# Kernel optimization log

Measured on AMD Instinct MI355X. Metric: run time of the kernel, lower is better.

## Reference

```python
import jax, jax.numpy as jnp
import numpy as np

DIM, FFN, GC, NSET, K = 48, 2, 2, 32, 3
HID = DIM * FFN          # 96 hidden features
G = HID // GC            # 48 groups in KBA
CG = HID // G            # 2 channels per group
INTERC = 24              # min(dim, 24)
B, H, W = 4, 128, 128


def _conv(x, w, b=None, groups=1, pad=0):
    out = jax.lax.conv_general_dilated(
        x, w, (1, 1), [(pad, pad), (pad, pad)],
        dimension_numbers=('NCHW', 'OIHW', 'NCHW'),
        feature_group_count=groups)
    if b is not None:
        out = out + b[None, :, None, None]
    return out


def _kba(x, att, k, g, bb, ww):
    # x: [B,c,H,W], att: [B,nset,H,W], bb: [1,nset,c], ww: [1,nset,c*c//g*k*k]
    Bz, c, Hh, Ww = x.shape
    KK = k * k
    cg = c // g
    P = Hh * Ww
    a = att.reshape(Bz, -1, P).transpose(0, 2, 1)                     # [B,P,nset]
    bias = jnp.einsum('bpn,nc->bpc', a, bb[0])                        # [B,P,c]
    attk = jnp.einsum('bpn,nm->bpm', a, ww[0]).reshape(Bz, P, g, cg, cg * KK)
    pd = k // 2
    xp = jnp.pad(x, ((0, 0), (0, 0), (pd, pd), (pd, pd)))
    # im2col patches, torch.unfold layout: channel-major, kernel row-major
    patches = jnp.stack([xp[:, :, i:i + Hh, j:j + Ww]
                         for i in range(k) for j in range(k)], axis=2)  # [B,c,KK,H,W]
    uf = patches.reshape(Bz, g, cg * KK, P).transpose(0, 3, 1, 2)       # [B,P,g,cg*KK]
    out = jnp.einsum('bpgom,bpgm->bpgo', attk, uf).reshape(Bz, P, c) + bias
    return out.transpose(0, 2, 1).reshape(Bz, c, Hh, Ww)


def setup_inputs() -> dict:
    key = jax.random.key(0)
    ks = jax.random.split(key, 20)
    s = 0.05
    inp = {
        'x': jax.random.normal(ks[0], (B, DIM, H, W), jnp.float32),
        'dw1_w': jax.random.normal(ks[1], (HID, DIM, 1, 1), jnp.float32) * s,
        'dw2_w': jax.random.normal(ks[2], (HID, 1, 3, 3), jnp.float32) * s,
        'proj_w': jax.random.normal(ks[3], (DIM, HID, 1, 1), jnp.float32) * s,
        'sca_w': jax.random.normal(ks[4], (HID, HID, 1, 1), jnp.float32) * s,
        'sca_b': jax.random.normal(ks[5], (HID,), jnp.float32) * s,
        'c1_w1': jax.random.normal(ks[6], (HID, DIM, 1, 1), jnp.float32) * s,
        'c1_w2': jax.random.normal(ks[7], (HID, 1, 3, 3), jnp.float32) * s,
        'kba_w': jax.random.normal(ks[8], (1, NSET, HID * CG * K * K), jnp.float32) * s,
        'kba_b': jax.random.normal(ks[9], (1, NSET, HID), jnp.float32) * s,
        'c2_w1': jax.random.normal(ks[10], (INTERC, DIM // INTERC, 3, 3), jnp.float32) * s,
        'c2_b1': jax.random.normal(ks[11], (INTERC,), jnp.float32) * s,
        'c2_w2': jax.random.normal(ks[12], (NSET, INTERC // 2, 1, 1), jnp.float32) * s,
        'c2_b2': jax.random.normal(ks[13], (NSET,), jnp.float32) * s,
        'c211_w': jax.random.normal(ks[14], (NSET, DIM, 1, 1), jnp.float32) * s,
        'c211_b': jax.random.normal(ks[15], (NSET,), jnp.float32) * s,
        'attgamma': jnp.full((1, NSET, 1, 1), 0.01, jnp.float32),
        'ga1': jnp.full((1, HID, 1, 1), 0.01, jnp.float32),
    }
    return inp


def reference(x, dw1_w, dw2_w, proj_w, sca_w, sca_b, c1_w1, c1_w2,
              kba_w, kba_b, c2_w1, c2_b1, c2_w2, c2_b2,
              c211_w, c211_b, attgamma, ga1):
    # dwconv branch: 1x1 -> depthwise 3x3
    x1 = _conv(_conv(x, dw1_w), dw2_w, groups=HID, pad=1)
    # attention map branch: grouped 3x3 -> SimpleGate -> 1x1, scaled + skip 1x1
    t = _conv(x, c2_w1, c2_b1, groups=INTERC, pad=1)
    t1, t2 = jnp.split(t, 2, axis=1)
    t = _conv(t1 * t2, c2_w2, c2_b2)
    att = t * attgamma + _conv(x, c211_w, c211_b)
    # conv1 branch feeding KBA
    uf = _conv(_conv(x, c1_w1), c1_w2, groups=HID, pad=1)
    x2 = _kba(uf, att, K, G, kba_b, kba_w) * ga1 + uf
    comb = jax.nn.gelu(x1, approximate=False) * x2
    pooled = jnp.mean(comb, axis=(2, 3), keepdims=True)
    comb = comb * _conv(pooled, sca_w, sca_b)
    return _conv(comb, proj_w)
```

## Files before the change

### kernel.cpp

```cpp
#include <hip/hip_runtime.h>
#include <math.h>

#define BB 4
#define HH 128
#define WW 128
#define HWP (HH*WW)
#define DIMC 48
#define HIDC 96
#define NSETC 32

typedef __attribute__((ext_vector_type(8))) short bf16x8;
typedef __attribute__((ext_vector_type(4))) float f32x4;
typedef __attribute__((ext_vector_type(2))) float f32x2;

static __device__ __forceinline__ unsigned short f2bf(float f) {
    union { float f; unsigned u; } v; v.f = f;
    unsigned r = (v.u + 0x7FFFu + ((v.u >> 16) & 1u)) >> 16;
    return (unsigned short)r;
}
static __device__ __forceinline__ unsigned rnd_bf(float f) {
    union { float f; unsigned u; } v; v.f = f;
    return v.u + 0x8000u;
}
static __device__ __forceinline__ unsigned pack2bf(float lo, float hi) {
    return __builtin_amdgcn_perm(rnd_bf(hi), rnd_bf(lo), 0x07060302u);
}
static __device__ __forceinline__ void st_bf_hi(unsigned short* p, float f) {
    *p = (unsigned short)(rnd_bf(f) >> 16);
}
static __device__ __forceinline__ float bf2f(unsigned short u) {
    union { unsigned u; float f; } v; v.u = ((unsigned)u) << 16;
    return v.f;
}
static __device__ __forceinline__ float bfpair_lo(unsigned pr) {
    union { unsigned u; float f; } v; v.u = pr << 16; return v.f;
}
static __device__ __forceinline__ float bfpair_hi(unsigned pr) {
    union { unsigned u; float f; } v; v.u = pr & 0xffff0000u; return v.f;
}
static __device__ __forceinline__ float gelu(float x) {
    return 0.5f * x * (1.0f + erff(x * 0.70710678118654752f));
}

__global__ __launch_bounds__(256) void k_prep(
    const float* __restrict__ x,
    const float* __restrict__ kbaw, const float* __restrict__ kbab,
    const float* __restrict__ dw1w, const float* __restrict__ c1w1,
    const float* __restrict__ ga1,  const float* __restrict__ c211w,
    const float* __restrict__ c2w2, const float* __restrict__ c2b2,
    const float* __restrict__ c211b, const float* __restrict__ attg,
    unsigned short* __restrict__ Bpk, unsigned short* __restrict__ Bpw,
    unsigned short* __restrict__ Aps, unsigned short* __restrict__ Ag,
    unsigned* __restrict__ x_p, float* __restrict__ pooled)
{
    __shared__ unsigned ts[256 * 26];
    int blk = blockIdx.x, tid = threadIdx.x;
    if (blk < 300) {
        int t = blk * 256 + tid;
        if (t < 61440) {
            int j = t & 7, lane = (t >> 3) & 63, tile = t >> 9;
            int chunk = tile / 10, nt = tile - chunk * 10;
            int m = lane & 15, qn = lane >> 4;
            int lc = 4 * nt + (m & 3);
            int o = lc / 20, tt = lc % 20;
            int c = (m >> 2) * 24 + 2 * chunk + o;
            int n = qn * 8 + j;
            float v = 0.f;
            if (tt < 18)       v = kbaw[n * 1728 + (c >> 1) * 36 + (c & 1) * 18 + tt] * ga1[c];
            else if (tt == 18) v = kbab[n * 96 + c] * ga1[c];
            Bpk[t] = f2bf(v);
        } else if (t < 73728) {
            int u = t - 61440;
            int s = u / 6144;
            int rem = u % 6144;
            int nt = rem >> 9;
            int lane = (rem >> 3) & 63, j = rem & 7;
            int k = s * 32 + ((lane >> 4) << 3) + j;
            int col = (nt << 4) + (lane & 15);
            float v = 0.f;
            if (k < 48) v = (col < 96) ? dw1w[col * 48 + k] : c1w1[(col - 96) * 48 + k];
            Bpw[u] = f2bf(v);
        } else if (t < 75776) {
            int u = t - 73728;
            int j = u & 7, lane = (u >> 3) & 63, tile = u >> 9;
            int kt = tile >> 1, nt2 = tile & 1;
            int m = lane & 15, qn = lane >> 4;
            int n = 8 * (m >> 2) + 4 * nt2 + (m & 3);
            int k = kt * 32 + qn * 8 + j;
            Aps[u] = f2bf(k < 48 ? c211w[n * 48 + k] : 0.f);
        } else if (t < 76800) {
            int u = t - 75776;
            int j = u & 7, lane = (u >> 3) & 63, nt2 = u >> 9;
            int m = lane & 15, qn = lane >> 4;
            int n = 8 * (m >> 2) + 4 * nt2 + (m & 3);
            int k = qn * 8 + j;
            float v = 0.f;
            if (k < 12)       v = c2w2[n * 12 + k] * attg[n];
            else if (k == 12) v = c2b2[n] * attg[n] + c211b[n];
            Ag[u] = f2bf(v);
        }
    } else {
        int xblk = blk - 300;
        if (xblk == 0) {
            for (int i = tid; i < BB * HIDC; i += 256) pooled[i] = 0.f;
        }
        int b = xblk >> 6;
        int p0 = (xblk & 63) << 8;
        const float* xb = x + (size_t)b * DIMC * HWP + p0;
        #pragma unroll
        for (int c2 = 0; c2 < 24; ++c2) {
            float lo = xb[(2 * c2) * HWP + tid];
            float hi = xb[(2 * c2 + 1) * HWP + tid];
            ts[tid * 26 + c2] = pack2bf(lo, hi);
        }
        __syncthreads();
        unsigned* dst = x_p + ((size_t)b * HWP + p0) * 24;
        for (int idx = tid; idx < 256 * 24; idx += 256) {
            int px = idx / 24, j2 = idx - px * 24;
            dst[px * 24 + j2] = ts[px * 26 + j2];
        }
    }
}

__global__ __launch_bounds__(512, 4) void k_mff(
    const unsigned* __restrict__ x_p,
    const uint4* __restrict__ BpkA, const uint4* __restrict__ Bpw,
    const uint4* __restrict__ Aps,  const uint4* __restrict__ Ag,
    const float* __restrict__ c1w2, const float* __restrict__ dw2w,
    const float* __restrict__ c2w1, const float* __restrict__ c2b1,
    unsigned* __restrict__ comb_bf, float* __restrict__ pooled)
{
    __shared__ __attribute__((aligned(16))) unsigned xs[144 * 26];
    __shared__ __attribute__((aligned(16))) unsigned short hsw[144 * 100];
    __shared__ unsigned short us2p[100 * 100];
    __shared__ float wls[864 + 432 + 24];
    __shared__ float pooled_s[96];

    int lane = threadIdx.x, wy = threadIdx.y;
    int tid = wy * 64 + lane;
    int blk = blockIdx.x;
    int b = blk >> 8, ty = (blk >> 4) & 15, tx = blk & 15;
    int q = lane >> 4, i16 = lane & 15;
    int wh = wy >> 2;
    int wp = wy & 3;

    float* wats  = wls + 864;
    float* c2b1s = wls + 864 + 432;
    float* att_tf = (float*)hsw;

    if (tid < 96) pooled_s[tid] = 0.f;
    for (int idx = tid; idx < 864; idx += 512) {
        int t5 = idx / 96, c = idx - t5 * 96;
        wls[idx] = dw2w[c * 9 + t5];
    }
    for (int idx = tid; idx < 216; idx += 512) {
        int g = idx / 9, tap = idx - g * 9;
        wats[idx * 2]     = c2w1[g * 18 + tap];
        wats[idx * 2 + 1] = c2w1[g * 18 + 9 + tap];
    }
    if (tid < 24) c2b1s[tid] = c2b1[tid];
    for (int idx = tid; idx < 144 * 12; idx += 512) {
        int pos = idx / 12, jp = idx - pos * 12;
        int gy = ty * 8 - 2 + pos / 12, gx = tx * 8 - 2 + pos % 12;
        uint2 v = {0u, 0u};
        if (((unsigned)gy < (unsigned)HH) & ((unsigned)gx < (unsigned)WW))
            v = *(const uint2*)&x_p[((size_t)b * HWP + gy * WW + gx) * 24 + jp * 2];
        *(uint2*)&xs[pos * 26 + jp * 2] = v;
    }
    __syncthreads();

    int p_t = wp * 16 + i16;
    int pyT = p_t >> 3, pxT = p_t & 7;
    int gp = (ty * 8 + pyT) * WW + tx * 8 + pxT;
    uint4 z4 = {0u, 0u, 0u, 0u};

    #pragma unroll
    for (int ci = 0; ci < 3; ++ci) {
        int g = q * 6 + wh * 3 + ci;
        float acc = c2b1s[g];
        #pragma unroll
        for (int di = 0; di < 3; ++di)
          #pragma unroll
          for (int dj = 0; dj < 3; ++dj) {
              unsigned pr = xs[((pyT + 1 + di) * 12 + pxT + 1 + dj) * 26 + g];
              f32x2 w2 = *(const f32x2*)&wats[(g * 9 + di * 3 + dj) * 2];
              acc += w2.x * bfpair_lo(pr) + w2.y * bfpair_hi(pr);
          }
        att_tf[p_t * 26 + g] = acc;
    }
    __syncthreads();

    bf16x8 afrag;
    {
        int p26 = p_t * 26;
        unsigned tgd[4];
        #pragma unroll
        for (int i2 = 0; i2 < 4; ++i2) {
            int k0 = q * 8 + 2 * i2;
            int k1 = k0 + 1;
            float v0 = (k0 < 12) ? att_tf[p26 + k0] * att_tf[p26 + 12 + k0] : (k0 == 12 ? 1.f : 0.f);
            float v1 = (k1 < 12) ? att_tf[p26 + k1] * att_tf[p26 + 12 + k1] : (k1 == 12 ? 1.f : 0.f);
            tgd[i2] = pack2bf(v0, v1);
        }
        uint4 tgr = {tgd[0], tgd[1], tgd[2], tgd[3]};
        bf16x8 btg = __builtin_bit_cast(bf16x8, tgr);

        int cen = (pyT + 2) * 12 + (pxT + 2);
        uint2 xa = *(const uint2*)&xs[cen * 26 + q * 4];
        uint2 xb2 = *(const uint2*)&xs[cen * 26 + q * 4 + 2];
        uint4 bx0r = {xa.x, xa.y, xb2.x, xb2.y};
        uint4 bx1r = z4;
        if (q < 2) {
            uint2 xc = *(const uint2*)&xs[cen * 26 + 16 + q * 4];
            uint2 xd = *(const uint2*)&xs[cen * 26 + 16 + q * 4 + 2];
            bx1r.x = xc.x; bx1r.y = xc.y; bx1r.z = xd.x; bx1r.w = xd.y;
        }
        bf16x8 bx0 = __builtin_bit_cast(bf16x8, bx0r);
        bf16x8 bx1 = __builtin_bit_cast(bf16x8, bx1r);

        float attv[8];
        #pragma unroll
        for (int nt2 = 0; nt2 < 2; ++nt2) {
            bf16x8 ag  = __builtin_bit_cast(bf16x8, Ag[nt2 * 64 + lane]);
            bf16x8 as0 = __builtin_bit_cast(bf16x8, Aps[nt2 * 64 + lane]);
            bf16x8 as1 = __builtin_bit_cast(bf16x8, Aps[(2 + nt2) * 64 + lane]);
            f32x4 z = {0.f, 0.f, 0.f, 0.f};
            f32x4 c = __builtin_amdgcn_mfma_f32_16x16x32_bf16(ag, btg, z, 0, 0, 0);
            c = __builtin_amdgcn_mfma_f32_16x16x32_bf16(as1, bx1, c, 0, 0, 0);
            c = __builtin_amdgcn_mfma_f32_16x16x32_bf16(as0, bx0, c, 0, 0, 0);
            #pragma unroll
            for (int r = 0; r < 4; ++r) attv[nt2 * 4 + r] = c[r];
        }
        uint4 au = {pack2bf(attv[0], attv[1]), pack2bf(attv[2], attv[3]),
                    pack2bf(attv[4], attv[5]), pack2bf(attv[6], attv[7])};
        afrag = __builtin_bit_cast(bf16x8, au);
    }
    __syncthreads();

    {
        int nA = (wy == 0) ? 2 : 1;
        #pragma unroll 1
        for (int rr = 0; rr < nA; ++rr) {
            int rg = rr ? 8 : wy;
            int hp = rg * 16 + i16;
            uint2 xa = *(const uint2*)&xs[hp * 26 + q * 4];
            uint2 xb2 = *(const uint2*)&xs[hp * 26 + q * 4 + 2];
            uint4 a0r = {xa.x, xa.y, xb2.x, xb2.y};
            uint4 a1r = z4;
            if (q < 2) {
                uint2 xc = *(const uint2*)&xs[hp * 26 + 16 + q * 4];
                uint2 xd = *(const uint2*)&xs[hp * 26 + 16 + q * 4 + 2];
                a1r.x = xc.x; a1r.y = xc.y; a1r.z = xd.x; a1r.w = xd.y;
            }
            bf16x8 a0 = __builtin_bit_cast(bf16x8, a0r);
            bf16x8 a1 = __builtin_bit_cast(bf16x8, a1r);
            int rowb = rg * 16 + 4 * q;
            #pragma unroll
            for (int nt = 0; nt < 6; ++nt) {
                bf16x8 b0 = __builtin_bit_cast(bf16x8, Bpw[(size_t)((6 + nt) << 6) + lane]);
                bf16x8 b1 = __builtin_bit_cast(bf16x8, Bpw[(size_t)((18 + nt) << 6) + lane]);
                f32x4 z = {0.f, 0.f, 0.f, 0.f};
                f32x4 c = __builtin_amdgcn_mfma_f32_16x16x32_bf16(a1, b1, z, 0, 0, 0);
                c = __builtin_amdgcn_mfma_f32_16x16x32_bf16(a0, b0, c, 0, 0, 0);
                #pragma unroll
                for (int r = 0; r < 4; ++r)
                    st_bf_hi(&hsw[(rowb + r) * 100 + nt * 16 + i16], c[r]);
            }
        }
    }
    __syncthreads();

    #pragma unroll 1
    for (int it = 0; it < 3; ++it) {
        int su = wy * 3 + it;
        int cq = su >> 1;
        const float* w9 = c1w2 + cq * 8 * 9;
        int hp2 = (su & 1) * 50 + lane;
        if (lane < 50) {
            int py2 = hp2 / 10, px2 = hp2 - py2 * 10;
            float acc[8];
            #pragma unroll
            for (int c = 0; c < 8; ++c) acc[c] = 0.f;
            #pragma unroll
            for (int di = 0; di < 3; ++di)
              #pragma unroll
              for (int dj = 0; dj < 3; ++dj) {
                  int row = (py2 + di) * 12 + px2 + dj;
                  uint2 v0 = *(const uint2*)&hsw[row * 100 + cq * 8];
                  uint2 v1 = *(const uint2*)&hsw[row * 100 + cq * 8 + 4];
                  unsigned pp[4] = {v0.x, v0.y, v1.x, v1.y};
                  #pragma unroll
                  for (int c2 = 0; c2 < 4; ++c2) {
                      acc[2*c2]   += w9[(2*c2) * 9 + di * 3 + dj]   * bfpair_lo(pp[c2]);
                      acc[2*c2+1] += w9[(2*c2+1) * 9 + di * 3 + dj] * bfpair_hi(pp[c2]);
                  }
              }
            uint2 o0, o1;
            o0.x = pack2bf(acc[0], acc[1]);
            o0.y = pack2bf(acc[2], acc[3]);
            o1.x = pack2bf(acc[4], acc[5]);
            o1.y = pack2bf(acc[6], acc[7]);
            *(uint2*)&us2p[hp2 * 100 + cq * 8]     = o0;
            *(uint2*)&us2p[hp2 * 100 + cq * 8 + 4] = o1;
        }
    }
    __syncthreads();

    if (wy < 7) {
        int rg = wy;
        int hp = rg * 16 + i16;
        bool okp = hp < 100;
        int hy = hp / 10, hx = hp - hy * 10;
        int pos = okp ? ((hy + 1) * 12 + hx + 1) : 0;
        uint2 xa = *(const uint2*)&xs[pos * 26 + q * 4];
        uint2 xb2 = *(const uint2*)&xs[pos * 26 + q * 4 + 2];
        uint4 a0r = {xa.x, xa.y, xb2.x, xb2.y};
        uint4 a1r = z4;
        if (q < 2) {
            uint2 xc = *(const uint2*)&xs[pos * 26 + 16 + q * 4];
            uint2 xd = *(const uint2*)&xs[pos * 26 + 16 + q * 4 + 2];
            a1r.x = xc.x; a1r.y = xc.y; a1r.z = xd.x; a1r.w = xd.y;
        }
        bf16x8 a0 = __builtin_bit_cast(bf16x8, a0r);
        bf16x8 a1 = __builtin_bit_cast(bf16x8, a1r);
        int rowb = rg * 16 + 4 * q;
        #pragma unroll
        for (int nt = 0; nt < 6; ++nt) {
            bf16x8 b0 = __builtin_bit_cast(bf16x8, Bpw[(size_t)(nt << 6) + lane]);
            bf16x8 b1 = __builtin_bit_cast(bf16x8, Bpw[(size_t)((12 + nt) << 6) + lane]);
            f32x4 z = {0.f, 0.f, 0.f, 0.f};
            f32x4 c = __builtin_amdgcn_mfma_f32_16x16x32_bf16(a1, b1, z, 0, 0, 0);
            c = __builtin_amdgcn_mfma_f32_16x16x32_bf16(a0, b0, c, 0, 0, 0);
            #pragma unroll
            for (int r = 0; r < 4; ++r)
                st_bf_hi(&hsw[(rowb + r) * 100 + nt * 16 + i16], c[r]);
        }
    }
    __syncthreads();

    f32x2 greg[6];
    {
        int base = q * 24 + wh * 12;
        #pragma unroll
        for (int cc = 0; cc < 6; ++cc) {
            int c0 = base + 2 * cc;
            f32x2 acc = {0.f, 0.f};
            #pragma unroll
            for (int di = 0; di < 3; ++di)
              #pragma unroll
              for (int dj = 0; dj < 3; ++dj) {
                  unsigned pr = *(const unsigned*)&hsw[((pyT + di) * 10 + pxT + dj) * 100 + c0];
                  f32x2 hv = {bfpair_lo(pr), bfpair_hi(pr)};
                  f32x2 wv = *(const f32x2*)&wls[(di * 3 + dj) * 96 + c0];
                  acc += wv * hv;
              }
            greg[cc].x = gelu(acc.x);
            greg[cc].y = gelu(acc.y);
        }
    }

    unsigned* cmb = comb_bf + ((size_t)b * HWP + gp) * 48 + q * 12;
    int hpC = (pyT + 1) * 10 + pxT + 1;

    #pragma unroll
    for (int cl = 0; cl < 6; ++cl) {
        int chunk = wh * 6 + cl;
        f32x4 cf[10];
        #pragma unroll
        for (int nt = 0; nt < 10; ++nt) {
            bf16x8 aW = __builtin_bit_cast(bf16x8, BpkA[(size_t)((chunk * 10 + nt) << 6) + lane]);
            f32x4 z = {0.f, 0.f, 0.f, 0.f};
            cf[nt] = __builtin_amdgcn_mfma_f32_16x16x32_bf16(aW, afrag, z, 0, 0, 0);
        }
        int c0 = q * 24 + 2 * chunk;
        float u[18];
        #pragma unroll
        for (int i = 0; i < 3; ++i)
          #pragma unroll
          for (int j = 0; j < 3; ++j) {
              unsigned pr = *(const unsigned*)&us2p[((pyT + i) * 10 + pxT + j) * 100 + c0];
              u[i * 3 + j]     = bfpair_lo(pr);
              u[9 + i * 3 + j] = bfpair_hi(pr);
          }
        float acc0 = cf[4][2];
        float acc1 = cf[9][2];
        #pragma unroll
        for (int m = 0; m < 16; ++m) {
            acc0 += cf[m >> 2][m & 3]       * u[m];
            acc1 += cf[5 + (m >> 2)][m & 3] * u[m];
        }
        acc0 += cf[4][0] * u[16] + cf[4][1] * u[17];
        acc1 += cf[9][0] * u[16] + cf[9][1] * u[17];

        unsigned sp = *(const unsigned*)&us2p[hpC * 100 + c0];
        float x20 = acc0 + bfpair_lo(sp);
        float x21 = acc1 + bfpair_hi(sp);
        float cv0 = greg[cl].x * x20;
        float cv1 = greg[cl].y * x21;
        cmb[chunk] = pack2bf(cv0, cv1);
        float r0 = cv0, r1 = cv1;
        #pragma unroll
        for (int s = 1; s < 16; s <<= 1) {
            r0 += __shfl_xor(r0, s, 64);
            r1 += __shfl_xor(r1, s, 64);
        }
        if (i16 == 0) {
            atomicAdd(&pooled_s[c0], r0);
            atomicAdd(&pooled_s[c0 + 1], r1);
        }
    }
    __syncthreads();
    if (tid < 96) atomicAdd(&pooled[b * HIDC + tid], pooled_s[tid]);
}

__global__ __launch_bounds__(256) void k_final(
    const unsigned* __restrict__ comb_bf, const float* __restrict__ pooled,
    const float* __restrict__ scaw, const float* __restrict__ scab,
    const float* __restrict__ projw, float* __restrict__ out)
{
    __shared__ float svs[96];
    __shared__ float cs[96][66];
    int tid = threadIdx.x;
    int blk = blockIdx.x;
    int p0 = blk * 64;
    int b = p0 >> 14;
    if (tid < 96) {
        float dot = 0.f;
        const float* pr = pooled + b * 96;
        const float* wr = scaw + tid * 96;
        #pragma unroll 4
        for (int k = 0; k < 96; ++k) dot += wr[k] * pr[k];
        svs[tid] = scab[tid] + dot * (1.0f / (float)HWP);
    }
    __syncthreads();
    for (int idx = tid; idx < 64 * 12; idx += 256) {
        int px = idx / 12, cq = idx - px * 12;
        uint4 v = *(const uint4*)&comb_bf[(size_t)(p0 + px) * 48 + cq * 4];
        int k0 = cq * 8;
        unsigned pp[4] = {v.x, v.y, v.z, v.w};
        #pragma unroll
        for (int j = 0; j < 4; ++j) {
            cs[k0 + 2*j][px]     = bfpair_lo(pp[j]) * svs[k0 + 2*j];
            cs[k0 + 2*j + 1][px] = bfpair_hi(pp[j]) * svs[k0 + 2*j + 1];
        }
    }
    __syncthreads();
    int l = tid & 63, w = tid >> 6;
    int o0 = w * 12;
    float acc[12];
    #pragma unroll
    for (int o = 0; o < 12; ++o) acc[o] = 0.f;
    #pragma unroll 4
    for (int k = 0; k < 96; ++k) {
        float v = cs[k][l];
        #pragma unroll
        for (int o = 0; o < 12; ++o)
            acc[o] += projw[(o0 + o) * 96 + k] * v;
    }
    float* ob = out + (size_t)b * DIMC * HWP + (p0 & 16383) + l;
    #pragma unroll
    for (int o = 0; o < 12; ++o)
        ob[(o0 + o) * HWP] = acc[o];
}

extern "C" void kernel_launch(void* const* d_in, const int* in_sizes, int n_in,
                              void* d_out, int out_size, void* d_ws, size_t ws_size,
                              hipStream_t stream)
{
    const float* x     = (const float*)d_in[0];
    const float* dw1w  = (const float*)d_in[1];
    const float* dw2w  = (const float*)d_in[2];
    const float* projw = (const float*)d_in[3];
    const float* scaw  = (const float*)d_in[4];
    const float* scab  = (const float*)d_in[5];
    const float* c1w1  = (const float*)d_in[6];
    const float* c1w2  = (const float*)d_in[7];
    const float* kbaw  = (const float*)d_in[8];
    const float* kbab  = (const float*)d_in[9];
    const float* c2w1  = (const float*)d_in[10];
    const float* c2b1  = (const float*)d_in[11];
    const float* c2w2  = (const float*)d_in[12];
    const float* c2b2  = (const float*)d_in[13];
    const float* c211w = (const float*)d_in[14];
    const float* c211b = (const float*)d_in[15];
    const float* attg  = (const float*)d_in[16];
    const float* ga1   = (const float*)d_in[17];

    unsigned* x_p     = (unsigned*)d_ws;
    unsigned* comb_bf = x_p + (size_t)BB * HWP * 24;
    float* pooled     = (float*)(comb_bf + (size_t)BB * HWP * 48);
    unsigned short* BpkA = (unsigned short*)(pooled + BB * HIDC);
    unsigned short* Bpw  = BpkA + 61440;
    unsigned short* Aps  = Bpw + 12288;
    unsigned short* Ag   = Aps + 2048;

    k_prep <<<556,  256, 0, stream>>>(x, kbaw, kbab, dw1w, c1w1, ga1, c211w, c2w2, c2b2,
                                      c211b, attg, BpkA, Bpw, Aps, Ag, x_p, pooled);
    k_mff  <<<1024, dim3(64,8,1), 0, stream>>>(x_p, (const uint4*)BpkA, (const uint4*)Bpw,
                                               (const uint4*)Aps, (const uint4*)Ag,
                                               c1w2, dw2w, c2w1, c2b1, comb_bf, pooled);
    k_final<<<1024, 256, 0, stream>>>(comb_bf, pooled, scaw, scab, projw, (float*)d_out);
}
```

Before: 206.1 us.

## Pad shared-memory row strides to odd words and relax launch bounds

Changes the LDS row strides (xs 26→27 words, hsw/us2p 100→102 halves, i.e. 51 words) to avoid bank conflicts, replacing the vector uint2 LDS accesses with scalar 32-bit accesses that the new alignment requires. It lowers the launch-bounds minimum blocks from 4 to 2, giving the compiler more registers per thread at possible occupancy cost. It also hoists the us2p neighbourhood loads ahead of the MFMA batch so LDS latency overlaps the matrix ops. The risk is more LDS instructions from the scalarized accesses, plus lower occupancy.

New measurement: 200.8 us. -2.5%, faster.

```diff
diff --git a/kernel.cpp b/kernel.cpp
--- a/kernel.cpp
+++ b/kernel.cpp
@@ -8,6 +8,10 @@
 #define DIMC 48
 #define HIDC 96
 #define NSETC 32
+
+#define XS_W 27
+#define HS_W 102
+#define US_W 102
 
 typedef __attribute__((ext_vector_type(8))) short bf16x8;
 typedef __attribute__((ext_vector_type(4))) float f32x4;
@@ -122,7 +126,7 @@
     }
 }
 
-__global__ __launch_bounds__(512, 4) void k_mff(
+__global__ __launch_bounds__(512, 2) void k_mff(
     const unsigned* __restrict__ x_p,
     const uint4* __restrict__ BpkA, const uint4* __restrict__ Bpw,
     const uint4* __restrict__ Aps,  const uint4* __restrict__ Ag,
@@ -130,9 +134,9 @@
     const float* __restrict__ c2w1, const float* __restrict__ c2b1,
     unsigned* __restrict__ comb_bf, float* __restrict__ pooled)
 {
-    __shared__ __attribute__((aligned(16))) unsigned xs[144 * 26];
-    __shared__ __attribute__((aligned(16))) unsigned short hsw[144 * 100];
-    __shared__ unsigned short us2p[100 * 100];
+    __shared__ __attribute__((aligned(16))) unsigned xs[144 * XS_W];
+    __shared__ __attribute__((aligned(16))) unsigned short hsw[144 * HS_W];
+    __shared__ unsigned short us2p[100 * US_W];
     __shared__ float wls[864 + 432 + 24];
     __shared__ float pooled_s[96];
 
@@ -165,7 +169,8 @@
         uint2 v = {0u, 0u};
         if (((unsigned)gy < (unsigned)HH) & ((unsigned)gx < (unsigned)WW))
             v = *(const uint2*)&x_p[((size_t)b * HWP + gy * WW + gx) * 24 + jp * 2];
-        *(uint2*)&xs[pos * 26 + jp * 2] = v;
+        xs[pos * XS_W + jp * 2]     = v.x;
+        xs[pos * XS_W + jp * 2 + 1] = v.y;
     }
     __syncthreads();
 
@@ -182,17 +187,17 @@
         for (int di = 0; di < 3; ++di)
           #pragma unroll
           for (int dj = 0; dj < 3; ++dj) {
-              unsigned pr = xs[((pyT + 1 + di) * 12 + pxT + 1 + dj) * 26 + g];
+              unsigned pr = xs[((pyT + 1 + di) * 12 + pxT + 1 + dj) * XS_W + g];
               f32x2 w2 = *(const f32x2*)&wats[(g * 9 + di * 3 + dj) * 2];
               acc += w2.x * bfpair_lo(pr) + w2.y * bfpair_hi(pr);
           }
-        att_tf[p_t * 26 + g] = acc;
+        att_tf[p_t * XS_W + g] = acc;
     }
     __syncthreads();
 
     bf16x8 afrag;
     {
-        int p26 = p_t * 26;
+        int p26 = p_t * XS_W;
         unsigned tgd[4];
         #pragma unroll
         for (int i2 = 0; i2 < 4; ++i2) {
@@ -206,14 +211,12 @@
         bf16x8 btg = __builtin_bit_cast(bf16x8, tgr);
 
         int cen = (pyT + 2) * 12 + (pxT + 2);
-        uint2 xa = *(const uint2*)&xs[cen * 26 + q * 4];
-        uint2 xb2 = *(const uint2*)&xs[cen * 26 + q * 4 + 2];
-        uint4 bx0r = {xa.x, xa.y, xb2.x, xb2.y};
+        int cb = cen * XS_W + q * 4;
+        uint4 bx0r = {xs[cb], xs[cb + 1], xs[cb + 2], xs[cb + 3]};
         uint4 bx1r = z4;
         if (q < 2) {
-            uint2 xc = *(const uint2*)&xs[cen * 26 + 16 + q * 4];
-            uint2 xd = *(const uint2*)&xs[cen * 26 + 16 + q * 4 + 2];
-            bx1r.x = xc.x; bx1r.y = xc.y; bx1r.z = xd.x; bx1r.w = xd.y;
+            int cb2 = cen * XS_W + 16 + q * 4;
+            bx1r.x = xs[cb2]; bx1r.y = xs[cb2 + 1]; bx1r.z = xs[cb2 + 2]; bx1r.w = xs[cb2 + 3];
         }
         bf16x8 bx0 = __builtin_bit_cast(bf16x8, bx0r);
         bf16x8 bx1 = __builtin_bit_cast(bf16x8, bx1r);
@@ -243,14 +246,12 @@
         for (int rr = 0; rr < nA; ++rr) {
             int rg = rr ? 8 : wy;
             int hp = rg * 16 + i16;
-            uint2 xa = *(const uint2*)&xs[hp * 26 + q * 4];
-            uint2 xb2 = *(const uint2*)&xs[hp * 26 + q * 4 + 2];
-            uint4 a0r = {xa.x, xa.y, xb2.x, xb2.y};
+            int ab = hp * XS_W + q * 4;
+            uint4 a0r = {xs[ab], xs[ab + 1], xs[ab + 2], xs[ab + 3]};
             uint4 a1r = z4;
             if (q < 2) {
-                uint2 xc = *(const uint2*)&xs[hp * 26 + 16 + q * 4];
-                uint2 xd = *(const uint2*)&xs[hp * 26 + 16 + q * 4 + 2];
-                a1r.x = xc.x; a1r.y = xc.y; a1r.z = xd.x; a1r.w = xd.y;
+                int ab2 = hp * XS_W + 16 + q * 4;
+                a1r.x = xs[ab2]; a1r.y = xs[ab2 + 1]; a1r.z = xs[ab2 + 2]; a1r.w = xs[ab2 + 3];
             }
             bf16x8 a0 = __builtin_bit_cast(bf16x8, a0r);
             bf16x8 a1 = __builtin_bit_cast(bf16x8, a1r);
@@ -264,7 +265,7 @@
                 c = __builtin_amdgcn_mfma_f32_16x16x32_bf16(a0, b0, c, 0, 0, 0);
                 #pragma unroll
                 for (int r = 0; r < 4; ++r)
-                    st_bf_hi(&hsw[(rowb + r) * 100 + nt * 16 + i16], c[r]);
+                    st_bf_hi(&hsw[(rowb + r) * HS_W + nt * 16 + i16], c[r]);
             }
         }
     }
@@ -285,23 +286,23 @@
             for (int di = 0; di < 3; ++di)
               #pragma unroll
               for (int dj = 0; dj < 3; ++dj) {
-                  int row = (py2 + di) * 12 + px2 + dj;
-                  uint2 v0 = *(const uint2*)&hsw[row * 100 + cq * 8];
-                  uint2 v1 = *(const uint2*)&hsw[row * 100 + cq * 8 + 4];
-                  unsigned pp[4] = {v0.x, v0.y, v1.x, v1.y};
+                  int rb = ((py2 + di) * 12 + px2 + dj) * HS_W + cq * 8;
+                  unsigned pp[4];
+                  pp[0] = *(const unsigned*)&hsw[rb];
+                  pp[1] = *(const unsigned*)&hsw[rb + 2];
+                  pp[2] = *(const unsigned*)&hsw[rb + 4];
+                  pp[3] = *(const unsigned*)&hsw[rb + 6];
                   #pragma unroll
                   for (int c2 = 0; c2 < 4; ++c2) {
                       acc[2*c2]   += w9[(2*c2) * 9 + di * 3 + dj]   * bfpair_lo(pp[c2]);
                       acc[2*c2+1] += w9[(2*c2+1) * 9 + di * 3 + dj] * bfpair_hi(pp[c2]);
                   }
               }
-            uint2 o0, o1;
-            o0.x = pack2bf(acc[0], acc[1]);
-            o0.y = pack2bf(acc[2], acc[3]);
-            o1.x = pack2bf(acc[4], acc[5]);
-            o1.y = pack2bf(acc[6], acc[7]);
-            *(uint2*)&us2p[hp2 * 100 + cq * 8]     = o0;
-            *(uint2*)&us2p[hp2 * 100 + cq * 8 + 4] = o1;
+            int wb = hp2 * US_W + cq * 8;
+            *(unsigned*)&us2p[wb]     = pack2bf(acc[0], acc[1]);
+            *(unsigned*)&us2p[wb + 2] = pack2bf(acc[2], acc[3]);
+            *(unsigned*)&us2p[wb + 4] = pack2bf(acc[4], acc[5]);
+            *(unsigned*)&us2p[wb + 6] = pack2bf(acc[6], acc[7]);
         }
     }
     __syncthreads();
@@ -312,14 +313,12 @@
         bool okp = hp < 100;
         int hy = hp / 10, hx = hp - hy * 10;
         int pos = okp ? ((hy + 1) * 12 + hx + 1) : 0;
-        uint2 xa = *(const uint2*)&xs[pos * 26 + q * 4];
-        uint2 xb2 = *(const uint2*)&xs[pos * 26 + q * 4 + 2];
-        uint4 a0r = {xa.x, xa.y, xb2.x, xb2.y};
+        int ab = pos * XS_W + q * 4;
+        uint4 a0r = {xs[ab], xs[ab + 1], xs[ab + 2], xs[ab + 3]};
         uint4 a1r = z4;
         if (q < 2) {
-            uint2 xc = *(const uint2*)&xs[pos * 26 + 16 + q * 4];
-            uint2 xd = *(const uint2*)&xs[pos * 26 + 16 + q * 4 + 2];
-            a1r.x = xc.x; a1r.y = xc.y; a1r.z = xd.x; a1r.w = xd.y;
+            int ab2 = pos * XS_W + 16 + q * 4;
+            a1r.x = xs[ab2]; a1r.y = xs[ab2 + 1]; a1r.z = xs[ab2 + 2]; a1r.w = xs[ab2 + 3];
         }
         bf16x8 a0 = __builtin_bit_cast(bf16x8, a0r);
         bf16x8 a1 = __builtin_bit_cast(bf16x8, a1r);
@@ -333,7 +332,7 @@
             c = __builtin_amdgcn_mfma_f32_16x16x32_bf16(a0, b0, c, 0, 0, 0);
             #pragma unroll
             for (int r = 0; r < 4; ++r)
-                st_bf_hi(&hsw[(rowb + r) * 100 + nt * 16 + i16], c[r]);
+                st_bf_hi(&hsw[(rowb + r) * HS_W + nt * 16 + i16], c[r]);
         }
     }
     __syncthreads();
@@ -349,7 +348,7 @@
             for (int di = 0; di < 3; ++di)
               #pragma unroll
               for (int dj = 0; dj < 3; ++dj) {
-                  unsigned pr = *(const unsigned*)&hsw[((pyT + di) * 10 + pxT + dj) * 100 + c0];
+                  unsigned pr = *(const unsigned*)&hsw[((pyT + di) * 10 + pxT + dj) * HS_W + c0];
                   f32x2 hv = {bfpair_lo(pr), bfpair_hi(pr)};
                   f32x2 wv = *(const f32x2*)&wls[(di * 3 + dj) * 96 + c0];
                   acc += wv * hv;
@@ -365,6 +364,17 @@
     #pragma unroll
     for (int cl = 0; cl < 6; ++cl) {
         int chunk = wh * 6 + cl;
+        int c0 = q * 24 + 2 * chunk;
+        float u[18];
+        #pragma unroll
+        for (int i = 0; i < 3; ++i)
+          #pragma unroll
+          for (int j = 0; j < 3; ++j) {
+              unsigned pr = *(const unsigned*)&us2p[((pyT + i) * 10 + pxT + j) * US_W + c0];
+              u[i * 3 + j]     = bfpair_lo(pr);
+              u[9 + i * 3 + j] = bfpair_hi(pr);
+          }
+        unsigned sp = *(const unsigned*)&us2p[hpC * US_W + c0];
         f32x4 cf[10];
         #pragma unroll
         for (int nt = 0; nt < 10; ++nt) {
@@ -372,16 +382,6 @@
             f32x4 z = {0.f, 0.f, 0.f, 0.f};
             cf[nt] = __builtin_amdgcn_mfma_f32_16x16x32_bf16(aW, afrag, z, 0, 0, 0);
         }
-        int c0 = q * 24 + 2 * chunk;
-        float u[18];
-        #pragma unroll
-        for (int i = 0; i < 3; ++i)
-          #pragma unroll
-          for (int j = 0; j < 3; ++j) {
-              unsigned pr = *(const unsigned*)&us2p[((pyT + i) * 10 + pxT + j) * 100 + c0];
-              u[i * 3 + j]     = bfpair_lo(pr);
-              u[9 + i * 3 + j] = bfpair_hi(pr);
-          }
         float acc0 = cf[4][2];
         float acc1 = cf[9][2];
         #pragma unroll
@@ -392,7 +392,6 @@
         acc0 += cf[4][0] * u[16] + cf[4][1] * u[17];
         acc1 += cf[9][0] * u[16] + cf[9][1] * u[17];
 
-        unsigned sp = *(const unsigned*)&us2p[hpC * 100 + c0];
         float x20 = acc0 + bfpair_lo(sp);
         float x21 = acc1 + bfpair_hi(sp);
         float cv0 = greg[cl].x * x20;
```
